# Kernel tuning notes

Hardware: AMD Instinct MI355X
Metric: run time of the kernel (lower is better)

## Reference

```python
import jax, jax.numpy as jnp
import numpy as np

B, H, W, N = 8, 384, 384, 96
STEPSZ = 0.1; ALPHA = 0.01; BETA = 0.01; STD = 1.0
NSTEPS = 50; NSTEPS_W = 10; DMAX = 15.0; EXTGRADFAC = 10.0

def make_gauss_edge_fltr(std):
    # Gaussian-derivative edge filters, one per spatial dim: [2,1,k,k]
    r = int(np.ceil(3 * std)); t = np.arange(-r, r + 1, dtype=np.float32)
    g = np.exp(-t * t / (2 * std * std)); g /= g.sum()
    dg = -t / (std * std) * np.exp(-t * t / (2 * std * std)); dg /= np.abs(dg).sum()
    fy = np.outer(dg, g)   # d/drow
    fx = np.outer(g, dg)   # d/dcol
    return np.stack([fy, fx])[:, None].astype(np.float32)

def setup_inputs() -> dict:
    key = jax.random.key(0)
    k1, k2 = jax.random.split(key, 2)
    pred_dmap = jax.random.normal(k1, (B, 1, H, W), jnp.float32)
    nodes = jax.random.uniform(k2, (B, N, 2), jnp.float32)
    nodes = nodes * jnp.array([H - 1.0, W - 1.0], jnp.float32)
    nodes = jnp.sort(nodes, axis=1)  # roughly monotone chain -> path-like snake
    widths = jnp.ones((B, N), jnp.float32) * 3.0
    fltr = jnp.asarray(make_gauss_edge_fltr(STD))
    return {"pred_dmap": pred_dmap, "nodes": nodes, "widths": widths, "fltr": fltr}

def grad_im(x, fltr):
    # x: [B,1,H,W], fltr: [2,1,k,k] -> [B,2,H,W]
    return jax.lax.conv_general_dilated(x, fltr, (1, 1), 'SAME',
                                        dimension_numbers=('NCHW', 'OIHW', 'NCHW'))

def interp(img, pts):
    # bilinear sample: img [C,H,W], pts [N,2] (row,col) -> [N,C]
    C, Hh, Ww = img.shape
    y = jnp.clip(pts[:, 0], 0.0, Hh - 1.0); x = jnp.clip(pts[:, 1], 0.0, Ww - 1.0)
    y0 = jnp.floor(y).astype(jnp.int32); x0 = jnp.floor(x).astype(jnp.int32)
    y1 = jnp.minimum(y0 + 1, Hh - 1); x1 = jnp.minimum(x0 + 1, Ww - 1)
    wy = y - y0; wx = x - x0
    v00 = img[:, y0, x0]; v01 = img[:, y0, x1]
    v10 = img[:, y1, x0]; v11 = img[:, y1, x1]
    v = v00 * (1 - wy) * (1 - wx) + v01 * (1 - wy) * wx + v10 * wy * (1 - wx) + v11 * wy * wx
    return v.T

def d2_open(x):
    # second difference with replicated endpoints (open snake)
    xp = jnp.concatenate([x[:1], x, x[-1:]], 0)
    return xp[:-2] - 2 * xp[1:-1] + xp[2:]

def snake_one(nodes, widths, g, gw):
    # explicit active-contour iterations on node positions
    def pstep(x, _):
        fext = interp(g, x)                       # [N,2] external force
        d2 = d2_open(x); d4 = d2_open(d2)
        return x + STEPSZ * (ALPHA * d2 - BETA * d4 + fext), None
    x, _ = jax.lax.scan(pstep, nodes, None, length=NSTEPS)
    # unit normals from central-difference tangents
    t = jnp.concatenate([x[1:2] - x[0:1], 0.5 * (x[2:] - x[:-2]), x[-1:] - x[-2:-1]], 0)
    n = jnp.stack([-t[:, 1], t[:, 0]], 1)
    n = n / (jnp.linalg.norm(n, axis=1, keepdims=True) + 1e-6)
    def wstep(w, _):
        gp = interp(gw, x + w[:, None] * n); gm = interp(gw, x - w[:, None] * n)
        f = 0.5 * (jnp.sum(gp * n, 1) - jnp.sum(gm * n, 1))
        return jnp.maximum(w + STEPSZ * f, 0.5), None
    w, _ = jax.lax.scan(wstep, widths, None, length=NSTEPS_W)
    return x, w

def render(x, w):
    # distance-to-ribbon map, clipped at DMAX; only [HW,S] intermediates
    ys, xs = jnp.meshgrid(jnp.arange(H, dtype=jnp.float32),
                          jnp.arange(W, dtype=jnp.float32), indexing='ij')
    P = jnp.stack([ys.ravel(), xs.ravel()], 1)          # [HW,2]
    a = x[:-1]; ab = x[1:] - a                          # [S,2]
    denom = jnp.sum(ab * ab, 1) + 1e-8                  # [S]
    dotpa = P @ ab.T - jnp.sum(a * ab, 1)               # [HW,S] = (P-a).ab
    t = jnp.clip(dotpa / denom, 0.0, 1.0)
    pa2 = jnp.sum(P * P, 1)[:, None] - 2 * (P @ a.T) + jnp.sum(a * a, 1)  # |P-a|^2
    d = jnp.sqrt(jnp.maximum(pa2 - 2 * t * dotpa + t * t * denom, 0.0))
    ws = 0.5 * (w[:-1] + w[1:])                         # per-segment width
    dmap = jnp.min(jnp.maximum(d - ws, 0.0), axis=1)
    return jnp.minimum(dmap, DMAX).reshape(H, W)

def reference(pred_dmap, nodes, widths, fltr):
    gimg = grad_im(pred_dmap, fltr) * EXTGRADFAC          # [B,2,H,W]
    gimgW = grad_im(jnp.abs(pred_dmap), fltr) * EXTGRADFAC
    def per_sample(nd, wd, g, gw):
        x, w = snake_one(nd, wd, g, gw)
        return render(x, w)
    dm = jax.vmap(per_sample)(nodes, widths, gimg, gimgW)[:, None]  # [B,1,H,W]
    dm = jax.lax.stop_gradient(dm)   # snake_dm.detach() in the original
    return jnp.mean((pred_dmap - dm) ** 2)
```

## Files before the change

kernel.cpp:

```cpp
#include <hip/hip_runtime.h>
#include <math.h>

#define BB   8
#define HH   384
#define WW   384
#define NN   96
#define HWSZ (HH * WW)
#define NSEG (NN - 1)
#define SEGF 12
#define SEGPAD 1152
#define DMAXV 15.0f
#define ROWS_PER_BLK 12
#define NCHUNK (HH / ROWS_PER_BLK)
#define CROWS 12
#define CBANDS (HH / CROWS)
#define MAGICU 0x9E3779B9u

typedef unsigned long long u64;
typedef unsigned int u32;

__device__ inline void st_pair(float* p, float lo, float hi)
{
    u64 v = ((u64)__float_as_uint(hi) << 32) | (u64)__float_as_uint(lo);
    __hip_atomic_store((u64*)p, v, __ATOMIC_RELAXED, __HIP_MEMORY_SCOPE_AGENT);
}

__device__ inline float ld_f32_coh(const float* p)
{
    u32 v = __hip_atomic_load((u32*)p, __ATOMIC_RELAXED, __HIP_MEMORY_SCOPE_AGENT);
    return __uint_as_float(v);
}

#define WAIT_ALL() asm volatile("s_waitcnt vmcnt(0) lgkmcnt(0)" ::: "memory")

__device__ inline void lds_barrier()
{
    asm volatile("s_waitcnt lgkmcnt(0)" ::: "memory");
    __builtin_amdgcn_sched_barrier(0);
    __builtin_amdgcn_s_barrier();
    __builtin_amdgcn_sched_barrier(0);
}

__device__ inline void load_taps(const float* __restrict__ fltr,
                                 float* __restrict__ sg, float* __restrict__ sdg)
{
    int tid = threadIdx.x;
    if (tid < 7) {
        float s = 0.f;
#pragma unroll
        for (int i = 0; i < 7; ++i) s += fabsf(fltr[i * 7 + tid]);
        sg[tid] = s;
    } else if (tid < 14) {
        int r = tid - 7;
        float s = 0.f;
#pragma unroll
        for (int j = 0; j < 7; ++j) s += fltr[r * 7 + j];
        sdg[r] = s;
    }
    __syncthreads();
}

__global__ __launch_bounds__(384) void conv_fused(
    const float* __restrict__ pred, const float* __restrict__ fltr,
    float2* __restrict__ g2, float2* __restrict__ gw2)
{
    __shared__ float sg[7], sdg[7];
    load_taps(fltr, sg, sdg);

    int blk = blockIdx.x;
    int b = blk & 7;
    int band = blk >> 3;
    int y0 = band * CROWS;
    int x = threadIdx.x;
    const float* pb = pred + (size_t)b * HWSZ;
    bool xin = (x >= 3) && (x < WW - 3);

    float hg[7], hd[7], hga[7], hda[7];

#pragma unroll
    for (int q = 0; q < CROWS + 6; ++q) {
        float vg = 0.f, vd = 0.f, vga = 0.f, vda = 0.f;
        int r = y0 + q - 3;
        if (r >= 0 && r < HH) {
            const float* row = pb + r * WW;
            if (xin) {
#pragma unroll
                for (int k = 0; k < 7; ++k) {
                    float v  = row[x + k - 3];
                    float av = fabsf(v);
                    vg  = fmaf(v,  sg[k],  vg);
                    vd  = fmaf(v,  sdg[k], vd);
                    vga = fmaf(av, sg[k],  vga);
                    vda = fmaf(av, sdg[k], vda);
                }
            } else {
#pragma unroll
                for (int k = 0; k < 7; ++k) {
                    int ix = x + k - 3;
                    float v  = (ix >= 0 && ix < WW) ? row[ix] : 0.f;
                    float av = fabsf(v);
                    vg  = fmaf(v,  sg[k],  vg);
                    vd  = fmaf(v,  sdg[k], vd);
                    vga = fmaf(av, sg[k],  vga);
                    vda = fmaf(av, sdg[k], vda);
                }
            }
        }
        hg[q % 7] = vg; hd[q % 7] = vd; hga[q % 7] = vga; hda[q % 7] = vda;

        if (q >= 6) {
            int y = y0 + q - 6;
            float o0 = 0.f, o1 = 0.f, o2 = 0.f, o3 = 0.f;
#pragma unroll
            for (int j = 0; j < 7; ++j) {
                int s = (q - 6 + j) % 7;
                o0 = fmaf(hg[s],  sdg[j], o0);
                o1 = fmaf(hd[s],  sg[j],  o1);
                o2 = fmaf(hga[s], sdg[j], o2);
                o3 = fmaf(hda[s], sg[j],  o3);
            }
            size_t gi = (size_t)b * HWSZ + (size_t)y * WW + x;
            g2[gi]  = make_float2(o0 * 10.f, o1 * 10.f);
            gw2[gi] = make_float2(o2 * 10.f, o3 * 10.f);
        }
    }
}

__device__ inline float2 bilin2i(const float2* __restrict__ img, float py, float px)
{
    float y = fminf(fmaxf(py, 0.0f), (float)(HH - 1));
    float x = fminf(fmaxf(px, 0.0f), (float)(WW - 1));
    int y0 = (int)floorf(y);
    int x0 = (int)floorf(x);
    int y1 = min(y0 + 1, HH - 1);
    bool xedge = (x0 + 1 > WW - 1);
    float wy = y - (float)y0;
    float wx = x - (float)x0;
    float4 r0 = *(const float4*)(img + y0 * WW + x0);
    float4 r1 = *(const float4*)(img + y1 * WW + x0);
    float2 v00 = make_float2(r0.x, r0.y);
    float2 v01 = xedge ? v00 : make_float2(r0.z, r0.w);
    float2 v10 = make_float2(r1.x, r1.y);
    float2 v11 = xedge ? v10 : make_float2(r1.z, r1.w);
    float w00 = (1.f - wy) * (1.f - wx);
    float w01 = (1.f - wy) * wx;
    float w10 = wy * (1.f - wx);
    float w11 = wy * wx;
    return make_float2(v00.x * w00 + v01.x * w01 + v10.x * w10 + v11.x * w11,
                       v00.y * w00 + v01.y * w01 + v10.y * w10 + v11.y * w11);
}

__device__ inline void write_seg_wt(float* __restrict__ r,
                                    float py, float px, float qy, float qx, float wseg)
{
    float aby = qy - py, abx = qx - px;
    float denom = aby * aby + abx * abx + 1e-8f;
    float aab = py * aby + px * abx;
    float aa  = py * py + px * px;
    float reach = DMAXV + wseg;
    st_pair(r + 0,  py,  px);
    st_pair(r + 2,  aby, abx);
    st_pair(r + 4,  aab, denom);
    st_pair(r + 6,  1.0f / denom, aa);
    st_pair(r + 8,  wseg, fminf(py, qy) - reach);
    st_pair(r + 10, fmaxf(py, qy) + reach, 0.f);
}

__global__ __launch_bounds__(384) void snake_render(
    const float* __restrict__ pred, const float* __restrict__ nodes,
    const float* __restrict__ widths,
    const float* __restrict__ g2f, const float* __restrict__ gw2f,
    float* __restrict__ segs, u64* __restrict__ pflag,
    u32* __restrict__ segflag, float* __restrict__ out)
{
    __shared__ float ss[NSEG * SEGF];
    __shared__ float2 posb[2][NN];
    __shared__ float  wbuf[NN];
    __shared__ int slo, shi;
    __shared__ float swsum[6];

    int blk = blockIdx.x;
    int b   = blk & 7;
    int band = blk >> 3;
    int t = threadIdx.x;

    int y0r = band * ROWS_PER_BLK;
    const float* pb = pred + (size_t)b * HWSZ + (size_t)y0r * WW + t;
    float pv[ROWS_PER_BLK];
#pragma unroll
    for (int ry = 0; ry < ROWS_PER_BLK; ++ry) pv[ry] = pb[ry * WW];

    if (t == 0) { slo = NSEG; shi = -1; }

    if (blk < 8) {
        const float2* gb  = (const float2*)g2f  + (size_t)b * HWSZ;
        const float2* gwb = (const float2*)gw2f + (size_t)b * HWSZ;
        int wv = t >> 6, ln = t & 63;
        int n  = wv * 48 + ln;
        bool act = (wv < 2) && (ln < 48);
        bool n0f = (n == 0), nlf = (n == NN - 1);

        float py = 0.f, px = 0.f;
        float4 r0 = make_float4(0.f, 0.f, 0.f, 0.f), r1 = r0;
        float wy = 0.f, wx = 0.f;
        bool xedge = false;

        if (act) {
            float2 p0 = *(const float2*)(nodes + (size_t)(b * NN + n) * 2);
            py = p0.x; px = p0.y;
            posb[0][n] = p0;
            float yc = fminf(fmaxf(py, 0.0f), (float)(HH - 1));
            float xc = fminf(fmaxf(px, 0.0f), (float)(WW - 1));
            int y0i = (int)floorf(yc);
            int x0i = (int)floorf(xc);
            int y1i = min(y0i + 1, HH - 1);
            xedge = (x0i + 1 > WW - 1);
            wy = yc - (float)y0i;
            wx = xc - (float)x0i;
            r0 = *(const float4*)(gb + y0i * WW + x0i);
            r1 = *(const float4*)(gb + y1i * WW + x0i);
        }
        lds_barrier();

        for (int s = 0; s < 50; ++s) {
            const float2* pcur = posb[s & 1];
            float2* pnxt = posb[(s & 1) ^ 1];
            if (act) {
                float2 xm1 = pcur[max(n - 1, 0)];
                float2 xp1 = pcur[min(n + 1, NN - 1)];
                float2 xm2 = pcur[max(n - 2, 0)];
                float2 xp2 = pcur[min(n + 2, NN - 1)];

                float d2m_y = xm2.x - 2.f * xm1.x + py;
                float d2c_y = xm1.x - 2.f * py + xp1.x;
                float d2p_y = py - 2.f * xp1.x + xp2.x;
                float d2m_x = xm2.y - 2.f * xm1.y + px;
                float d2c_x = xm1.y - 2.f * px + xp1.y;
                float d2p_x = px - 2.f * xp1.y + xp2.y;
                d2m_y = n0f ? d2c_y : d2m_y;
                d2m_x = n0f ? d2c_x : d2m_x;
                d2p_y = nlf ? d2c_y : d2p_y;
                d2p_x = nlf ? d2c_x : d2p_x;
                float d4_y = d2m_y - 2.f * d2c_y + d2p_y;
                float d4_x = d2m_x - 2.f * d2c_x + d2p_x;

                float2 v00 = make_float2(r0.x, r0.y);
                float2 v01 = xedge ? v00 : make_float2(r0.z, r0.w);
                float2 v10 = make_float2(r1.x, r1.y);
                float2 v11 = xedge ? v10 : make_float2(r1.z, r1.w);
                float w00 = (1.f - wy) * (1.f - wx);
                float w01 = (1.f - wy) * wx;
                float w10 = wy * (1.f - wx);
                float w11 = wy * wx;
                float fy = v00.x * w00 + v01.x * w01 + v10.x * w10 + v11.x * w11;
                float fx = v00.y * w00 + v01.y * w01 + v10.y * w10 + v11.y * w11;

                py += 0.1f * (0.01f * d2c_y - 0.01f * d4_y + fy);
                px += 0.1f * (0.01f * d2c_x - 0.01f * d4_x + fx);

                float yc = fminf(fmaxf(py, 0.0f), (float)(HH - 1));
                float xc = fminf(fmaxf(px, 0.0f), (float)(WW - 1));
                int y0i = (int)floorf(yc);
                int x0i = (int)floorf(xc);
                int y1i = min(y0i + 1, HH - 1);
                xedge = (x0i + 1 > WW - 1);
                wy = yc - (float)y0i;
                wx = xc - (float)x0i;
                r0 = *(const float4*)(gb + y0i * WW + x0i);
                r1 = *(const float4*)(gb + y1i * WW + x0i);

                pnxt[n] = make_float2(py, px);
            }
            lds_barrier();
        }

        float ny_ = 0.f, nx_ = 0.f, wn = 0.f;
        if (act) {
            float2 xm1 = posb[0][max(n - 1, 0)];
            float2 xp1 = posb[0][min(n + 1, NN - 1)];
            float ty, tx;
            if (n0f)      { ty = xp1.x - py;  tx = xp1.y - px; }
            else if (nlf) { ty = py - xm1.x;  tx = px - xm1.y; }
            else          { ty = 0.5f * (xp1.x - xm1.x); tx = 0.5f * (xp1.y - xm1.y); }

            float nn0 = -tx, nn1 = ty;
            float nrm = sqrtf(nn0 * nn0 + nn1 * nn1) + 1e-6f;
            ny_ = nn0 / nrm; nx_ = nn1 / nrm;

            wn = widths[b * NN + n];
            for (int s = 0; s < 10; ++s) {
                float2 gp = bilin2i(gwb, py + wn * ny_, px + wn * nx_);
                float2 gm = bilin2i(gwb, py - wn * ny_, px - wn * nx_);
                float fw = 0.5f * ((gp.x * ny_ + gp.y * nx_) - (gm.x * ny_ + gm.y * nx_));
                wn = fmaxf(wn + 0.1f * fw, 0.5f);
            }
            wbuf[n] = wn;
        }
        __syncthreads();

        if (act && n < NSEG) {
            float2 q = posb[0][n + 1];
            float wq = wbuf[n + 1];
            write_seg_wt(segs + (size_t)b * SEGPAD + (size_t)n * SEGF,
                         py, px, q.x, q.y, 0.5f * (wn + wq));
        }
        WAIT_ALL();
        __syncthreads();
        if (t == 0)
            __hip_atomic_store(&segflag[b], MAGICU,
                               __ATOMIC_RELAXED, __HIP_MEMORY_SCOPE_AGENT);
    } else {
        if (t == 0) {
            while (__hip_atomic_load(&segflag[b],
                                     __ATOMIC_RELAXED, __HIP_MEMORY_SCOPE_AGENT) != MAGICU)
                __builtin_amdgcn_s_sleep(8);
            asm volatile("" ::: "memory");
        }
    }

    __syncthreads();

    {
        int y0 = y0r;
        const float* sb = segs + (size_t)b * SEGPAD;
        for (int j = t; j < NSEG * SEGF; j += 384)
            ss[j] = ld_f32_coh(sb + j);
        __syncthreads();

        float cy0 = (float)y0, cy1 = (float)(y0 + ROWS_PER_BLK - 1);
        if (t < NSEG) {
            float ylo = ss[t * SEGF + 9];
            float yhi = ss[t * SEGF + 10];
            if (yhi >= cy0 && ylo <= cy1) {
                atomicMin(&slo, t);
                atomicMax(&shi, t);
            }
        }
        __syncthreads();
        int lo = slo, hi = shi;

        float px = (float)t;
        float px2 = px * px;
        float minv[ROWS_PER_BLK];
#pragma unroll
        for (int r = 0; r < ROWS_PER_BLK; ++r) minv[r] = DMAXV;

        for (int si = lo; si <= hi; ++si) {
            const float* r = ss + si * SEGF;
            float ax = r[1], abx = r[3], ws = r[8];
            float bxe = ax + abx;
            float reach = DMAXV + ws + 0.01f;
            if (px < fminf(ax, bxe) - reach || px > fmaxf(ax, bxe) + reach) continue;

            float ay = r[0], aby = r[2];
            float aab = r[4], denom = r[5], invd = r[6], aa = r[7];
            float dotpa_b = fmaf(px, abx, -aab);
            float pa2_b   = fmaf(px, -2.0f * ax, px2 + aa);
#pragma unroll
            for (int ry = 0; ry < ROWS_PER_BLK; ++ry) {
                float py = (float)(y0 + ry);
                float dotpa = fmaf(py, aby, dotpa_b);
                float tt = fminf(fmaxf(dotpa * invd, 0.0f), 1.0f);
                float pa2 = fmaf(py, fmaf(py, 1.0f, -2.0f * ay), pa2_b);
                float d2 = fmaf(tt, fmaf(tt, denom, -2.0f * dotpa), pa2);
                float d = sqrtf(fmaxf(d2, 0.0f));
                float v = fmaxf(d - ws, 0.0f);
                minv[ry] = fminf(minv[ry], v);
            }
        }

        float sq = 0.f;
#pragma unroll
        for (int ry = 0; ry < ROWS_PER_BLK; ++ry) {
            float diff = pv[ry] - minv[ry];
            sq = fmaf(diff, diff, sq);
        }

#pragma unroll
        for (int off = 32; off > 0; off >>= 1) sq += __shfl_down(sq, off, 64);
        if ((t & 63) == 0) swsum[t >> 6] = sq;
        __syncthreads();
        if (t == 0) {
            float tot = swsum[0] + swsum[1] + swsum[2] + swsum[3] + swsum[4] + swsum[5];
            u64 pvv = ((u64)MAGICU << 32) | (u64)__float_as_uint(tot);
            __hip_atomic_store(&pflag[blk], pvv,
                               __ATOMIC_RELAXED, __HIP_MEMORY_SCOPE_AGENT);
        }
    }

    if (blk == 8) {
        __syncthreads();
        float v = 0.f;
        if (t < 256) {
            u64 pvv = __hip_atomic_load(&pflag[t], __ATOMIC_RELAXED,
                                        __HIP_MEMORY_SCOPE_AGENT);
            while ((u32)(pvv >> 32) != MAGICU) {
                __builtin_amdgcn_s_sleep(4);
                pvv = __hip_atomic_load(&pflag[t], __ATOMIC_RELAXED,
                                        __HIP_MEMORY_SCOPE_AGENT);
            }
            v = __uint_as_float((u32)pvv);
        }
#pragma unroll
        for (int off = 32; off > 0; off >>= 1) v += __shfl_down(v, off, 64);
        if ((t & 63) == 0) swsum[t >> 6] = v;
        __syncthreads();
        if (t == 0) {
            float tot = swsum[0] + swsum[1] + swsum[2] + swsum[3] + swsum[4] + swsum[5];
            out[0] = tot * (1.0f / (float)(BB * HWSZ));
        }
    }
}

extern "C" void kernel_launch(void* const* d_in, const int* in_sizes, int n_in,
                              void* d_out, int out_size, void* d_ws, size_t ws_size,
                              hipStream_t stream)
{
    const float* pred   = (const float*)d_in[0];
    const float* nodes  = (const float*)d_in[1];
    const float* widths = (const float*)d_in[2];
    const float* fltr   = (const float*)d_in[3];
    float* out = (float*)d_out;

    float* ws   = (float*)d_ws;
    float* g2   = ws;
    float* gw2  = g2 + (size_t)2 * BB * HWSZ;
    float* segs = gw2 + (size_t)2 * BB * HWSZ;
    float* tail = segs + (size_t)BB * SEGPAD + 256;
    u64* pflag = (u64*)tail;
    u32* segflag = (u32*)(pflag + 256);

    conv_fused<<<BB * CBANDS, 384, 0, stream>>>(pred, fltr,
                                                (float2*)g2, (float2*)gw2);
    snake_render<<<BB * NCHUNK, 384, 0, stream>>>(pred, nodes, widths, g2, gw2,
                                                  segs, pflag, segflag, out);
}
```

Before: 118.8 us.

## Stage a 40-column band of gradient image around the snake path in LDS

The snake-step blocks now interpolate the initial node chain per image row to find a column center, then copy a 40-wide window of the gradient image (and later the width-gradient image) into shared memory. Bilinear samples during the 50 position steps and 10 width steps read from LDS when they fall inside the window, falling back to global loads otherwise. This targets the serial global-load latency on the critical path of the iterative snake, at the cost of about 120KB of LDS, a serial per-row search over the nodes, and two bulk copy phases.

```diff
diff --git a/kernel.cpp b/kernel.cpp
--- a/kernel.cpp
+++ b/kernel.cpp
@@ -15,6 +15,7 @@
 #define CROWS 12
 #define CBANDS (HH / CROWS)
 #define MAGICU 0x9E3779B9u
+#define W0 40
 
 typedef unsigned long long u64;
 typedef unsigned int u32;
@@ -124,30 +125,6 @@
             gw2[gi] = make_float2(o2 * 10.f, o3 * 10.f);
         }
     }
-}
-
-__device__ inline float2 bilin2i(const float2* __restrict__ img, float py, float px)
-{
-    float y = fminf(fmaxf(py, 0.0f), (float)(HH - 1));
-    float x = fminf(fmaxf(px, 0.0f), (float)(WW - 1));
-    int y0 = (int)floorf(y);
-    int x0 = (int)floorf(x);
-    int y1 = min(y0 + 1, HH - 1);
-    bool xedge = (x0 + 1 > WW - 1);
-    float wy = y - (float)y0;
-    float wx = x - (float)x0;
-    float4 r0 = *(const float4*)(img + y0 * WW + x0);
-    float4 r1 = *(const float4*)(img + y1 * WW + x0);
-    float2 v00 = make_float2(r0.x, r0.y);
-    float2 v01 = xedge ? v00 : make_float2(r0.z, r0.w);
-    float2 v10 = make_float2(r1.x, r1.y);
-    float2 v11 = xedge ? v10 : make_float2(r1.z, r1.w);
-    float w00 = (1.f - wy) * (1.f - wx);
-    float w01 = (1.f - wy) * wx;
-    float w10 = wy * (1.f - wx);
-    float w11 = wy * wx;
-    return make_float2(v00.x * w00 + v01.x * w01 + v10.x * w10 + v11.x * w11,
-                       v00.y * w00 + v01.y * w01 + v10.y * w10 + v11.y * w11);
 }
 
 __device__ inline void write_seg_wt(float* __restrict__ r,
@@ -173,11 +150,13 @@
     float* __restrict__ segs, u64* __restrict__ pflag,
     u32* __restrict__ segflag, float* __restrict__ out)
 {
-    __shared__ float ss[NSEG * SEGF];
+    __shared__ float2 LW[HH * W0];
     __shared__ float2 posb[2][NN];
     __shared__ float  wbuf[NN];
+    __shared__ short  cxw[HH];
     __shared__ int slo, shi;
     __shared__ float swsum[6];
+    float* ss = (float*)LW;
 
     int blk = blockIdx.x;
     int b   = blk & 7;
@@ -203,7 +182,8 @@
         float py = 0.f, px = 0.f;
         float4 r0 = make_float4(0.f, 0.f, 0.f, 0.f), r1 = r0;
         float wy = 0.f, wx = 0.f;
-        bool xedge = false;
+        bool pxe = false, inw = false;
+        int py0i = 0, py1i = 0, pl0 = 0, pl1 = 0;
 
         if (act) {
             float2 p0 = *(const float2*)(nodes + (size_t)(b * NN + n) * 2);
@@ -214,13 +194,72 @@
             int y0i = (int)floorf(yc);
             int x0i = (int)floorf(xc);
             int y1i = min(y0i + 1, HH - 1);
-            xedge = (x0i + 1 > WW - 1);
+            pxe = (x0i + 1 > WW - 1);
             wy = yc - (float)y0i;
             wx = xc - (float)x0i;
             r0 = *(const float4*)(gb + y0i * WW + x0i);
             r1 = *(const float4*)(gb + y1i * WW + x0i);
         }
         lds_barrier();
+
+        if (t < HH) {
+            float yy = (float)t;
+            float2 p0 = posb[0][0], plast = posb[0][NN - 1];
+            float xi;
+            if (yy <= p0.x) xi = p0.y;
+            else if (yy >= plast.x) xi = plast.y;
+            else {
+                int i = 0;
+                for (int k = 0; k < NN - 1; ++k)
+                    if (posb[0][k].x <= yy) i = k;
+                float2 a = posb[0][i], c = posb[0][i + 1];
+                xi = a.y + (c.y - a.y) * ((yy - a.x) / fmaxf(c.x - a.x, 1e-6f));
+            }
+            int cx = (int)xi - W0 / 2;
+            cxw[t] = (short)max(0, min(cx, WW - W0));
+        }
+        __syncthreads();
+
+        for (int idx = t; idx < HH * W0; idx += 384) {
+            int y = idx / W0;
+            int c = idx - y * W0;
+            LW[idx] = gb[y * WW + (int)cxw[y] + c];
+        }
+        __syncthreads();
+
+        auto bilinW = [&](const float2* __restrict__ img, float qy, float qx) -> float2 {
+            float y = fminf(fmaxf(qy, 0.0f), (float)(HH - 1));
+            float x = fminf(fmaxf(qx, 0.0f), (float)(WW - 1));
+            int y0i = (int)floorf(y);
+            int x0i = (int)floorf(x);
+            int y1i = min(y0i + 1, HH - 1);
+            bool xe = (x0i + 1 > WW - 1);
+            float fy = y - (float)y0i;
+            float fx = x - (float)x0i;
+            int l0 = x0i - (int)cxw[y0i];
+            int l1 = x0i - (int)cxw[y1i];
+            int lim = xe ? (W0 - 1) : (W0 - 2);
+            float2 v00, v01, v10, v11;
+            if (l0 >= 0 && l0 <= lim && l1 >= 0 && l1 <= lim) {
+                v00 = LW[y0i * W0 + l0];
+                v01 = xe ? v00 : LW[y0i * W0 + l0 + 1];
+                v10 = LW[y1i * W0 + l1];
+                v11 = xe ? v10 : LW[y1i * W0 + l1 + 1];
+            } else {
+                float4 q0 = *(const float4*)(img + y0i * WW + x0i);
+                float4 q1 = *(const float4*)(img + y1i * WW + x0i);
+                v00 = make_float2(q0.x, q0.y);
+                v01 = xe ? v00 : make_float2(q0.z, q0.w);
+                v10 = make_float2(q1.x, q1.y);
+                v11 = xe ? v10 : make_float2(q1.z, q1.w);
+            }
+            float w00 = (1.f - fy) * (1.f - fx);
+            float w01 = (1.f - fy) * fx;
+            float w10 = fy * (1.f - fx);
+            float w11 = fy * fx;
+            return make_float2(v00.x * w00 + v01.x * w01 + v10.x * w10 + v11.x * w11,
+                               v00.y * w00 + v01.y * w01 + v10.y * w10 + v11.y * w11);
+        };
 
         for (int s = 0; s < 50; ++s) {
             const float2* pcur = posb[s & 1];
@@ -244,10 +283,18 @@
                 float d4_y = d2m_y - 2.f * d2c_y + d2p_y;
                 float d4_x = d2m_x - 2.f * d2c_x + d2p_x;
 
-                float2 v00 = make_float2(r0.x, r0.y);
-                float2 v01 = xedge ? v00 : make_float2(r0.z, r0.w);
-                float2 v10 = make_float2(r1.x, r1.y);
-                float2 v11 = xedge ? v10 : make_float2(r1.z, r1.w);
+                float2 v00, v01, v10, v11;
+                if (inw) {
+                    v00 = LW[py0i * W0 + pl0];
+                    v01 = pxe ? v00 : LW[py0i * W0 + pl0 + 1];
+                    v10 = LW[py1i * W0 + pl1];
+                    v11 = pxe ? v10 : LW[py1i * W0 + pl1 + 1];
+                } else {
+                    v00 = make_float2(r0.x, r0.y);
+                    v01 = pxe ? v00 : make_float2(r0.z, r0.w);
+                    v10 = make_float2(r1.x, r1.y);
+                    v11 = pxe ? v10 : make_float2(r1.z, r1.w);
+                }
                 float w00 = (1.f - wy) * (1.f - wx);
                 float w01 = (1.f - wy) * wx;
                 float w10 = wy * (1.f - wx);
@@ -263,16 +310,32 @@
                 int y0i = (int)floorf(yc);
                 int x0i = (int)floorf(xc);
                 int y1i = min(y0i + 1, HH - 1);
-                xedge = (x0i + 1 > WW - 1);
+                bool xe = (x0i + 1 > WW - 1);
                 wy = yc - (float)y0i;
                 wx = xc - (float)x0i;
-                r0 = *(const float4*)(gb + y0i * WW + x0i);
-                r1 = *(const float4*)(gb + y1i * WW + x0i);
+                int l0 = x0i - (int)cxw[y0i];
+                int l1 = x0i - (int)cxw[y1i];
+                int lim = xe ? (W0 - 1) : (W0 - 2);
+                bool nin = (l0 >= 0) && (l0 <= lim) && (l1 >= 0) && (l1 <= lim);
+                if (!nin) {
+                    r0 = *(const float4*)(gb + y0i * WW + x0i);
+                    r1 = *(const float4*)(gb + y1i * WW + x0i);
+                }
+                inw = nin; pxe = xe;
+                py0i = y0i; py1i = y1i; pl0 = l0; pl1 = l1;
 
                 pnxt[n] = make_float2(py, px);
             }
             lds_barrier();
         }
+
+        __syncthreads();
+        for (int idx = t; idx < HH * W0; idx += 384) {
+            int y = idx / W0;
+            int c = idx - y * W0;
+            LW[idx] = gwb[y * WW + (int)cxw[y] + c];
+        }
+        __syncthreads();
 
         float ny_ = 0.f, nx_ = 0.f, wn = 0.f;
         if (act) {
@@ -289,8 +352,8 @@
 
             wn = widths[b * NN + n];
             for (int s = 0; s < 10; ++s) {
-                float2 gp = bilin2i(gwb, py + wn * ny_, px + wn * nx_);
-                float2 gm = bilin2i(gwb, py - wn * ny_, px - wn * nx_);
+                float2 gp = bilinW(gwb, py + wn * ny_, px + wn * nx_);
+                float2 gm = bilinW(gwb, py - wn * ny_, px - wn * nx_);
                 float fw = 0.5f * ((gp.x * ny_ + gp.y * nx_) - (gm.x * ny_ + gm.y * nx_));
                 wn = fmaxf(wn + 0.1f * fw, 0.5f);
             }
```

Result: slower. 155.5 us (+30.9%).

## Prefetch gradient rows near snake path into leader XCD's L2 while waiting

Applied to the files above, without the earlier changes.

The leader block of each batch writes its XCD id to a workspace flag. Idle waiting blocks on the same XCD read the nodes, estimate the snake's column for each row by interpolation, and touch a 64-column window of both gradient images around that path. The goal is to warm the L2 cache the snake iterations will hit, using time those blocks would otherwise spend spinning. This adds extra memory traffic and a second spin-wait, and the prefetch only helps if the snake stays inside the estimated window.

```diff
diff --git a/kernel.cpp b/kernel.cpp
--- a/kernel.cpp
+++ b/kernel.cpp
@@ -15,6 +15,8 @@
 #define CROWS 12
 #define CBANDS (HH / CROWS)
 #define MAGICU 0x9E3779B9u
+#define XTAG   0xA5A50000u
+#define XCCID_IMM 63508
 
 typedef unsigned long long u64;
 typedef unsigned int u32;
@@ -171,11 +173,14 @@
     const float* __restrict__ widths,
     const float* __restrict__ g2f, const float* __restrict__ gw2f,
     float* __restrict__ segs, u64* __restrict__ pflag,
-    u32* __restrict__ segflag, float* __restrict__ out)
+    u32* __restrict__ segflag, u32* __restrict__ xcdmap,
+    float* __restrict__ out)
 {
     __shared__ float ss[NSEG * SEGF];
     __shared__ float2 posb[2][NN];
     __shared__ float  wbuf[NN];
+    __shared__ short  cxw[HH];
+    __shared__ u32    sxm;
     __shared__ int slo, shi;
     __shared__ float swsum[6];
 
@@ -193,6 +198,12 @@
     if (t == 0) { slo = NSEG; shi = -1; }
 
     if (blk < 8) {
+        if (t == 0) {
+            u32 xid = __builtin_amdgcn_s_getreg(XCCID_IMM) & 0xFu;
+            __hip_atomic_store(&xcdmap[b], XTAG | xid,
+                               __ATOMIC_RELAXED, __HIP_MEMORY_SCOPE_AGENT);
+        }
+
         const float2* gb  = (const float2*)g2f  + (size_t)b * HWSZ;
         const float2* gwb = (const float2*)gw2f + (size_t)b * HWSZ;
         int wv = t >> 6, ln = t & 63;
@@ -311,6 +322,54 @@
                                __ATOMIC_RELAXED, __HIP_MEMORY_SCOPE_AGENT);
     } else {
         if (t == 0) {
+            u32 m;
+            while (((m = __hip_atomic_load(&xcdmap[b], __ATOMIC_RELAXED,
+                                           __HIP_MEMORY_SCOPE_AGENT))
+                    & 0xFFFF0000u) != XTAG)
+                __builtin_amdgcn_s_sleep(1);
+            sxm = m;
+        }
+        __syncthreads();
+        u32 myx = __builtin_amdgcn_s_getreg(XCCID_IMM) & 0xFu;
+        if ((sxm & 0xFu) == myx) {
+            for (int i = t; i < NN; i += 384)
+                posb[0][i] = *(const float2*)(nodes + (size_t)(b * NN + i) * 2);
+            __syncthreads();
+            for (int r = t; r < HH; r += 384) {
+                float yy = (float)r;
+                float2 p0 = posb[0][0], pl = posb[0][NN - 1];
+                float xi;
+                if (yy <= p0.x) xi = p0.y;
+                else if (yy >= pl.x) xi = pl.y;
+                else {
+                    int i = 0;
+                    for (int k = 0; k < NN - 1; ++k)
+                        if (posb[0][k].x <= yy) i = k;
+                    float2 a = posb[0][i], c = posb[0][i + 1];
+                    xi = a.y + (c.y - a.y) * ((yy - a.x) / fmaxf(c.x - a.x, 1e-6f));
+                }
+                int cx = ((int)xi - 32);
+                cxw[r] = (short)(max(0, min(cx, WW - 64)) & ~1);
+            }
+            __syncthreads();
+            const float2* gbp  = (const float2*)g2f  + (size_t)b * HWSZ;
+            const float2* gwbp = (const float2*)gw2f + (size_t)b * HWSZ;
+            int rank = band - 1;
+            float acc = 0.f;
+            if (t < 64) {
+                int pl2 = t >> 5, c = t & 31;
+                for (int r = rank; r < HH; r += 31) {
+                    int c0 = (int)cxw[r];
+                    const float4* w = pl2
+                        ? (const float4*)(gwbp + (size_t)r * WW + c0)
+                        : (const float4*)(gbp  + (size_t)r * WW + c0);
+                    float4 a = w[c];
+                    acc += a.x;
+                }
+            }
+            asm volatile("" :: "v"(acc));
+        }
+        if (t == 0) {
             while (__hip_atomic_load(&segflag[b],
                                      __ATOMIC_RELAXED, __HIP_MEMORY_SCOPE_AGENT) != MAGICU)
                 __builtin_amdgcn_s_sleep(8);
@@ -429,9 +488,11 @@
     float* tail = segs + (size_t)BB * SEGPAD + 256;
     u64* pflag = (u64*)tail;
     u32* segflag = (u32*)(pflag + 256);
+    u32* xcdmap  = segflag + 8;
 
     conv_fused<<<BB * CBANDS, 384, 0, stream>>>(pred, fltr,
                                                 (float2*)g2, (float2*)gw2);
     snake_render<<<BB * NCHUNK, 384, 0, stream>>>(pred, nodes, widths, g2, gw2,
-                                                  segs, pflag, segflag, out);
-}
+                                                  segs, pflag, segflag, xcdmap,
+                                                  out);
+}
```

Result: no change. 118.1 us (-0.6%).
